# Optimization experiments

Measured on AMD Instinct MI355X. Metric: run time of the kernel, lower is better.

Reference implementation:

```python
import jax, jax.numpy as jnp
import numpy as np


def _chamfer(samp_pc, ref_pc):
    """Squared-L2 chamfer: returns (cost_p1_p2 [B,N], cost_p2_p1 [B,M]).

    samp_pc: [B, N, 3], ref_pc: [B, M, 3]
    """
    s2 = jnp.sum(samp_pc * samp_pc, axis=-1)  # [B, N]
    r2 = jnp.sum(ref_pc * ref_pc, axis=-1)    # [B, M]
    cross = jnp.einsum('bnd,bmd->bnm', samp_pc, ref_pc)  # [B, N, M]
    d2 = s2[:, :, None] + r2[:, None, :] - 2.0 * cross   # [B, N, M]
    d2 = jnp.maximum(d2, 0.0)  # numerical floor
    cost_p1_p2 = jnp.min(d2, axis=2)  # [B, N] nearest ref for each samp point
    cost_p2_p1 = jnp.min(d2, axis=1)  # [B, M] nearest samp for each ref point
    return cost_p1_p2, cost_p2_p1


def setup_inputs() -> dict:
    key = jax.random.key(0)
    k1, k2 = jax.random.split(key)
    B, N, M = 16, 2048, 8192
    ref_pc = jax.random.normal(k1, (B, M, 3), dtype=jnp.float32)
    samp_pc = jax.random.normal(k2, (B, N, 3), dtype=jnp.float32)
    return {"ref_pc": ref_pc, "samp_pc": samp_pc}


def reference(ref_pc, samp_pc):
    cost_p1_p2, cost_p2_p1 = _chamfer(samp_pc, ref_pc)
    cd_p = (jnp.sqrt(cost_p1_p2).mean(axis=1) + jnp.sqrt(cost_p2_p1).mean(axis=1)) / 2.0
    cd_t = cost_p1_p2.mean(axis=1) + cost_p2_p1.mean(axis=1)
    return (cd_p, cd_t)
```

## Files before the change

### kernel.cpp

```cpp
#include <hip/hip_runtime.h>
#include <math.h>

#define BB 16
#define NN 2048
#define MM 8192

#define BLK 256
#define QSPL 2
#define NQ (NN / QSPL)
#define QSTG 256
#define NSTAGE (NQ / QSTG)
#define CTS (QSTG / 32)
#define YB (MM / 256)

typedef __attribute__((ext_vector_type(8))) short short8;
typedef __attribute__((ext_vector_type(16))) float f32x16;

union U16 { uint4 u; short8 s; };

static __device__ __forceinline__ unsigned short f2bf(float f) {
    unsigned int u = __float_as_uint(f);
    unsigned int r = (u + 0x7FFFu + ((u >> 16) & 1u)) >> 16;
    return (unsigned short)r;
}
static __device__ __forceinline__ float bf2f(unsigned short h) {
    return __uint_as_float(((unsigned int)h) << 16);
}

static __device__ __forceinline__ void glds16(const uint4* g, uint4* l) {
    __builtin_amdgcn_global_load_lds(
        (const __attribute__((address_space(1))) unsigned int*)g,
        (__attribute__((address_space(3))) unsigned int*)l,
        16, 0, 0);
}

#define DPP_MIN(v, CTRL)                                                      \
    v = fminf(v, __uint_as_float((unsigned)__builtin_amdgcn_update_dpp(       \
                     0, (int)__float_as_uint(v), CTRL, 0xF, 0xF, true)))
#define SWZ16_MIN(v)                                                          \
    v = fminf(v, __uint_as_float((unsigned)__builtin_amdgcn_ds_swizzle(       \
                     (int)__float_as_uint(v), 0x401F)))


__global__ void __launch_bounds__(BLK) prep_kernel(const float* __restrict__ samp,
                                                   unsigned short* __restrict__ Qpk) {
    const int i = blockIdx.x * BLK + threadIdx.x;
    const float* s0 = samp + (size_t)i * 3;
    float x = s0[0], y = s0[1], z = s0[2];
    float a5[5];
    a5[0] = x; a5[1] = y; a5[2] = z;
    a5[3] = 1.f; a5[4] = fmaf(x, x, fmaf(y, y, z * z));
    unsigned short h[3][5];
#pragma unroll
    for (int j = 0; j < 5; ++j) {
        float v = a5[j];
        h[0][j] = f2bf(v); float r1 = v - bf2f(h[0][j]);
        h[1][j] = f2bf(r1); float r2 = r1 - bf2f(h[1][j]);
        h[2][j] = f2bf(r2);
    }
    const int ordQ[6] = {0, 1, 0, 2, 0, 1};
    unsigned short K[32];
#pragma unroll
    for (int f = 0; f < 2; ++f) {
#pragma unroll
        for (int p2 = 0; p2 < 3; ++p2)
#pragma unroll
            for (int j2 = 0; j2 < 5; ++j2)
                K[f * 16 + p2 * 5 + j2] = h[ordQ[f * 3 + p2]][j2];
        K[f * 16 + 15] = 0;
    }
    unsigned int uu[16];
#pragma unroll
    for (int t = 0; t < 16; ++t)
        uu[t] = (unsigned int)K[2 * t] | ((unsigned int)K[2 * t + 1] << 16);
    uint4* dst = (uint4*)(Qpk + (size_t)i * 32);
    const int sw = (i >> 1) & 3;
    dst[0 ^ sw] = make_uint4(uu[0], uu[1], uu[2], uu[3]);
    dst[1 ^ sw] = make_uint4(uu[4], uu[5], uu[6], uu[7]);
    dst[2 ^ sw] = make_uint4(uu[8], uu[9], uu[10], uu[11]);
    dst[3 ^ sw] = make_uint4(uu[12], uu[13], uu[14], uu[15]);
}

__global__ void __launch_bounds__(BLK, 4) sweep_kernel(const float* __restrict__ ref,
                                                       const unsigned short* __restrict__ Qpk,
                                                       float* __restrict__ ws2p,
                                                       float* __restrict__ ws1p) {
    __shared__ uint4 Qt[2][QSTG * 4];
    __shared__ unsigned int qMin[NQ];

    const int b = blockIdx.x;
    const int m0 = blockIdx.y * 256;
    const int q0 = blockIdx.z * NQ;
    const int tid = threadIdx.x;
    const int w = tid >> 6;
    const int l = tid & 63;
    const int p = l & 31;
    const int kh = l >> 5;

    {
        const float* r0 = ref + ((size_t)(b * MM + m0 + tid)) * 3;
        float x = r0[0], y = r0[1], z = r0[2];
        float a5[5];
        a5[0] = -2.f * x; a5[1] = -2.f * y; a5[2] = -2.f * z;
        a5[3] = fmaf(x, x, fmaf(y, y, z * z)); a5[4] = 1.f;
        unsigned short h[3][5];
#pragma unroll
        for (int j = 0; j < 5; ++j) {
            float v = a5[j];
            h[0][j] = f2bf(v); float r1 = v - bf2f(h[0][j]);
            h[1][j] = f2bf(r1); float r2 = r1 - bf2f(h[1][j]);
            h[2][j] = f2bf(r2);
        }
        const int ordR[6] = {0, 0, 1, 0, 2, 1};
        unsigned short K[32];
#pragma unroll
        for (int f = 0; f < 2; ++f) {
#pragma unroll
            for (int p2 = 0; p2 < 3; ++p2)
#pragma unroll
                for (int j2 = 0; j2 < 5; ++j2)
                    K[f * 16 + p2 * 5 + j2] = h[ordR[f * 3 + p2]][j2];
            K[f * 16 + 15] = 0;
        }
        unsigned int uu[16];
#pragma unroll
        for (int t = 0; t < 16; ++t)
            uu[t] = (unsigned int)K[2 * t] | ((unsigned int)K[2 * t + 1] << 16);
        uint4* scr = &Qt[1][0];
        scr[0 * 256 + tid] = make_uint4(uu[0], uu[1], uu[2], uu[3]);
        scr[1 * 256 + tid] = make_uint4(uu[4], uu[5], uu[6], uu[7]);
        scr[2 * 256 + tid] = make_uint4(uu[8], uu[9], uu[10], uu[11]);
        scr[3 * 256 + tid] = make_uint4(uu[12], uu[13], uu[14], uu[15]);
    }
    for (int i = tid; i < NQ; i += BLK) qMin[i] = 0x7F7F7F7Fu;
    __syncthreads();

    U16 a0f0, a0f1, a1f0, a1f1;
    {
        const uint4* scr = &Qt[1][0];
        a0f0.u = scr[kh * 256 + w * 64 + p];
        a0f1.u = scr[(2 + kh) * 256 + w * 64 + p];
        a1f0.u = scr[kh * 256 + w * 64 + 32 + p];
        a1f1.u = scr[(2 + kh) * 256 + w * 64 + 32 + p];
    }

    const uint4* Q4 = (const uint4*)Qpk + ((size_t)b * NN + q0) * 4;
    {
        uint4* dst = &Qt[0][0];
#pragma unroll
        for (int k = 0; k < 4; ++k) glds16(Q4 + k * BLK + tid, dst + k * BLK + tid);
    }
    __syncthreads();

    float run0[16], run1[16];
#pragma unroll
    for (int j = 0; j < 16; ++j) { run0[j] = INFINITY; run1[j] = INFINITY; }

    const int sw = (p >> 1) & 3;
    const f32x16 fz = {0.f, 0.f, 0.f, 0.f, 0.f, 0.f, 0.f, 0.f,
                       0.f, 0.f, 0.f, 0.f, 0.f, 0.f, 0.f, 0.f};

    for (int st = 0; st < NSTAGE; ++st) {
        const uint4* qb = &Qt[st & 1][0];
        if (st < NSTAGE - 1) {
            const uint4* src = Q4 + (size_t)(st + 1) * (QSTG * 4);
            uint4* dst = &Qt[(st + 1) & 1][0];
#pragma unroll
            for (int k = 0; k < 4; ++k) glds16(src + k * BLK + tid, dst + k * BLK + tid);
        }
#pragma unroll 2
        for (int ct = 0; ct < CTS; ++ct) {
            const int pg = (ct * 32 + p) * 4;
            U16 b0, b1;
            b0.u = qb[pg + (kh ^ sw)];
            b1.u = qb[pg + ((2 + kh) ^ sw)];
            f32x16 d0 = __builtin_amdgcn_mfma_f32_32x32x16_bf16(a0f0.s, b0.s, fz, 0, 0, 0);
            d0 = __builtin_amdgcn_mfma_f32_32x32x16_bf16(a0f1.s, b1.s, d0, 0, 0, 0);
            f32x16 d1 = __builtin_amdgcn_mfma_f32_32x32x16_bf16(a1f0.s, b0.s, fz, 0, 0, 0);
            d1 = __builtin_amdgcn_mfma_f32_32x32x16_bf16(a1f1.s, b1.s, d1, 0, 0, 0);
#pragma unroll
            for (int j = 0; j < 16; ++j) {
                run0[j] = fminf(run0[j], d0[j]);
                run1[j] = fminf(run1[j], d1[j]);
            }
            float tv[8];
#pragma unroll
            for (int k = 0; k < 8; ++k) tv[k] = fminf(d0[k], d0[k + 8]);
#pragma unroll
            for (int k = 0; k < 8; ++k) tv[k] = fminf(tv[k], fminf(d1[k], d1[k + 8]));
#pragma unroll
            for (int k = 0; k < 4; ++k) tv[k] = fminf(tv[k], tv[k + 4]);
            float t = fminf(fminf(tv[0], tv[2]), fminf(tv[1], tv[3]));
            atomicMin(&qMin[st * QSTG + ct * 32 + p], __float_as_uint(fmaxf(t, 0.f)));
        }
        __syncthreads();
    }

    float* w1 = ws1p + ((size_t)blockIdx.y * BB + b) * NN + q0;
#pragma unroll
    for (int i = tid; i < NQ; i += BLK)
        w1[i] = __uint_as_float(qMin[i]);

#pragma unroll
    for (int j = 0; j < 16; ++j) {
        DPP_MIN(run0[j], 0xB1);  DPP_MIN(run0[j], 0x4E);
        DPP_MIN(run0[j], 0x141); DPP_MIN(run0[j], 0x140);
        SWZ16_MIN(run0[j]);
        DPP_MIN(run1[j], 0xB1);  DPP_MIN(run1[j], 0x4E);
        DPP_MIN(run1[j], 0x141); DPP_MIN(run1[j], 0x140);
        SWZ16_MIN(run1[j]);
    }
    float out = 0.f;
#pragma unroll
    for (int j = 0; j < 16; ++j) { if (p == j)      out = run0[j]; }
#pragma unroll
    for (int j = 0; j < 16; ++j) { if (p == 16 + j) out = run1[j]; }
    const int t2 = p >> 4, j4 = p & 15;
    const int row = t2 * 32 + (j4 & 3) + ((j4 >> 2) << 3) + 4 * kh;
    ws2p[((size_t)blockIdx.z * BB + b) * MM + m0 + w * 64 + row] = fmaxf(out, 0.f);
}

#define BLKR 1024
__global__ void __launch_bounds__(BLKR) reduce_kernel(const float* __restrict__ ws1p,
                                                      const float* __restrict__ ws2p,
                                                      float* __restrict__ out) {
    const int b = blockIdx.x;
    const int tid = threadIdx.x;
    const int lane = tid & 63;
    const int wv = tid >> 6;

    float sd1 = 0.f, sr1 = 0.f, sd2 = 0.f, sr2 = 0.f;
#pragma unroll
    for (int i = tid; i < NN; i += BLKR) {
        float m = INFINITY;
#pragma unroll
        for (int y = 0; y < YB; ++y)
            m = fminf(m, ws1p[((size_t)y * BB + b) * NN + i]);
        sd1 += m;
        sr1 += sqrtf(m);
    }
#pragma unroll
    for (int i = tid; i < MM; i += BLKR) {
        float v = fminf(ws2p[(size_t)b * MM + i],
                        ws2p[((size_t)BB + b) * MM + i]);
        sd2 += v;
        sr2 += sqrtf(v);
    }
#pragma unroll
    for (int s = 32; s > 0; s >>= 1) {
        sd1 += __shfl_xor(sd1, s);
        sr1 += __shfl_xor(sr1, s);
        sd2 += __shfl_xor(sd2, s);
        sr2 += __shfl_xor(sr2, s);
    }

    __shared__ float4 red[BLKR / 64];
    if (lane == 0) red[wv] = make_float4(sd1, sr1, sd2, sr2);
    __syncthreads();
    if (tid == 0) {
        float4 acc = red[0];
#pragma unroll
        for (int w = 1; w < BLKR / 64; ++w) {
            acc.x += red[w].x; acc.y += red[w].y;
            acc.z += red[w].z; acc.w += red[w].w;
        }
        out[b]      = (acc.y * (1.0f / NN) + acc.w * (1.0f / MM)) * 0.5f;
        out[BB + b] = acc.x * (1.0f / NN) + acc.z * (1.0f / MM);
    }
}

extern "C" void kernel_launch(void* const* d_in, const int* in_sizes, int n_in,
                              void* d_out, int out_size, void* d_ws, size_t ws_size,
                              hipStream_t stream) {
    const float* ref  = (const float*)d_in[0];
    const float* samp = (const float*)d_in[1];
    float* out = (float*)d_out;

    float* ws2p = (float*)d_ws;
    float* ws1p = ws2p + (size_t)QSPL * BB * MM;
    unsigned short* Qpk = (unsigned short*)(ws1p + (size_t)YB * BB * NN);

    prep_kernel<<<(BB * NN) / BLK, BLK, 0, stream>>>(samp, Qpk);

    dim3 gs(BB, MM / 256, QSPL);
    sweep_kernel<<<gs, BLK, 0, stream>>>(ref, Qpk, ws2p, ws1p);

    reduce_kernel<<<BB, BLKR, 0, stream>>>(ws1p, ws2p, out);
}
```

Measured before the change: 89.18 us.

## Fuse query packing into sweep kernel and split queries four ways

Measured after the change: 89.76 us. Within noise of the previous version (+0.7%).

```diff
diff --git a/kernel.cpp b/kernel.cpp
--- a/kernel.cpp
+++ b/kernel.cpp
@@ -6,11 +6,9 @@
 #define MM 8192
 
 #define BLK 256
-#define QSPL 2
+#define QSPL 4
 #define NQ (NN / QSPL)
-#define QSTG 256
-#define NSTAGE (NQ / QSTG)
-#define CTS (QSTG / 32)
+#define CTS (NQ / 32)
 #define YB (MM / 256)
 
 typedef __attribute__((ext_vector_type(8))) short short8;
@@ -27,11 +25,29 @@
     return __uint_as_float(((unsigned int)h) << 16);
 }
 
-static __device__ __forceinline__ void glds16(const uint4* g, uint4* l) {
-    __builtin_amdgcn_global_load_lds(
-        (const __attribute__((address_space(1))) unsigned int*)g,
-        (__attribute__((address_space(3))) unsigned int*)l,
-        16, 0, 0);
+static __device__ __forceinline__ void pack5(const float a5[5], const int ord[6],
+                                             unsigned int uu[16]) {
+    unsigned short h[3][5];
+#pragma unroll
+    for (int j = 0; j < 5; ++j) {
+        float v = a5[j];
+        h[0][j] = f2bf(v); float r1 = v - bf2f(h[0][j]);
+        h[1][j] = f2bf(r1); float r2 = r1 - bf2f(h[1][j]);
+        h[2][j] = f2bf(r2);
+    }
+    unsigned short K[32];
+#pragma unroll
+    for (int f = 0; f < 2; ++f) {
+#pragma unroll
+        for (int p2 = 0; p2 < 3; ++p2)
+#pragma unroll
+            for (int j2 = 0; j2 < 5; ++j2)
+                K[f * 16 + p2 * 5 + j2] = h[ord[f * 3 + p2]][j2];
+        K[f * 16 + 15] = 0;
+    }
+#pragma unroll
+    for (int t = 0; t < 16; ++t)
+        uu[t] = (unsigned int)K[2 * t] | ((unsigned int)K[2 * t + 1] << 16);
 }
 
 #define DPP_MIN(v, CTRL)                                                      \
@@ -42,50 +58,11 @@
                      (int)__float_as_uint(v), 0x401F)))
 
 
-__global__ void __launch_bounds__(BLK) prep_kernel(const float* __restrict__ samp,
-                                                   unsigned short* __restrict__ Qpk) {
-    const int i = blockIdx.x * BLK + threadIdx.x;
-    const float* s0 = samp + (size_t)i * 3;
-    float x = s0[0], y = s0[1], z = s0[2];
-    float a5[5];
-    a5[0] = x; a5[1] = y; a5[2] = z;
-    a5[3] = 1.f; a5[4] = fmaf(x, x, fmaf(y, y, z * z));
-    unsigned short h[3][5];
-#pragma unroll
-    for (int j = 0; j < 5; ++j) {
-        float v = a5[j];
-        h[0][j] = f2bf(v); float r1 = v - bf2f(h[0][j]);
-        h[1][j] = f2bf(r1); float r2 = r1 - bf2f(h[1][j]);
-        h[2][j] = f2bf(r2);
-    }
-    const int ordQ[6] = {0, 1, 0, 2, 0, 1};
-    unsigned short K[32];
-#pragma unroll
-    for (int f = 0; f < 2; ++f) {
-#pragma unroll
-        for (int p2 = 0; p2 < 3; ++p2)
-#pragma unroll
-            for (int j2 = 0; j2 < 5; ++j2)
-                K[f * 16 + p2 * 5 + j2] = h[ordQ[f * 3 + p2]][j2];
-        K[f * 16 + 15] = 0;
-    }
-    unsigned int uu[16];
-#pragma unroll
-    for (int t = 0; t < 16; ++t)
-        uu[t] = (unsigned int)K[2 * t] | ((unsigned int)K[2 * t + 1] << 16);
-    uint4* dst = (uint4*)(Qpk + (size_t)i * 32);
-    const int sw = (i >> 1) & 3;
-    dst[0 ^ sw] = make_uint4(uu[0], uu[1], uu[2], uu[3]);
-    dst[1 ^ sw] = make_uint4(uu[4], uu[5], uu[6], uu[7]);
-    dst[2 ^ sw] = make_uint4(uu[8], uu[9], uu[10], uu[11]);
-    dst[3 ^ sw] = make_uint4(uu[12], uu[13], uu[14], uu[15]);
-}
-
 __global__ void __launch_bounds__(BLK, 4) sweep_kernel(const float* __restrict__ ref,
-                                                       const unsigned short* __restrict__ Qpk,
+                                                       const float* __restrict__ samp,
                                                        float* __restrict__ ws2p,
                                                        float* __restrict__ ws1p) {
-    __shared__ uint4 Qt[2][QSTG * 4];
+    __shared__ uint4 Qf[4][NQ];
     __shared__ unsigned int qMin[NQ];
 
     const int b = blockIdx.x;
@@ -97,109 +74,84 @@
     const int p = l & 31;
     const int kh = l >> 5;
 
-    {
-        const float* r0 = ref + ((size_t)(b * MM + m0 + tid)) * 3;
-        float x = r0[0], y = r0[1], z = r0[2];
-        float a5[5];
-        a5[0] = -2.f * x; a5[1] = -2.f * y; a5[2] = -2.f * z;
-        a5[3] = fmaf(x, x, fmaf(y, y, z * z)); a5[4] = 1.f;
-        unsigned short h[3][5];
-#pragma unroll
-        for (int j = 0; j < 5; ++j) {
-            float v = a5[j];
-            h[0][j] = f2bf(v); float r1 = v - bf2f(h[0][j]);
-            h[1][j] = f2bf(r1); float r2 = r1 - bf2f(h[1][j]);
-            h[2][j] = f2bf(r2);
-        }
-        const int ordR[6] = {0, 0, 1, 0, 2, 1};
-        unsigned short K[32];
-#pragma unroll
-        for (int f = 0; f < 2; ++f) {
-#pragma unroll
-            for (int p2 = 0; p2 < 3; ++p2)
-#pragma unroll
-                for (int j2 = 0; j2 < 5; ++j2)
-                    K[f * 16 + p2 * 5 + j2] = h[ordR[f * 3 + p2]][j2];
-            K[f * 16 + 15] = 0;
-        }
-        unsigned int uu[16];
-#pragma unroll
-        for (int t = 0; t < 16; ++t)
-            uu[t] = (unsigned int)K[2 * t] | ((unsigned int)K[2 * t + 1] << 16);
-        uint4* scr = &Qt[1][0];
-        scr[0 * 256 + tid] = make_uint4(uu[0], uu[1], uu[2], uu[3]);
-        scr[1 * 256 + tid] = make_uint4(uu[4], uu[5], uu[6], uu[7]);
-        scr[2 * 256 + tid] = make_uint4(uu[8], uu[9], uu[10], uu[11]);
-        scr[3 * 256 + tid] = make_uint4(uu[12], uu[13], uu[14], uu[15]);
-    }
-    for (int i = tid; i < NQ; i += BLK) qMin[i] = 0x7F7F7F7Fu;
-    __syncthreads();
+    const int ordR[6] = {0, 0, 1, 0, 2, 1};
+    const int ordQ[6] = {0, 1, 0, 2, 0, 1};
 
     U16 a0f0, a0f1, a1f0, a1f1;
     {
-        const uint4* scr = &Qt[1][0];
-        a0f0.u = scr[kh * 256 + w * 64 + p];
-        a0f1.u = scr[(2 + kh) * 256 + w * 64 + p];
-        a1f0.u = scr[kh * 256 + w * 64 + 32 + p];
-        a1f1.u = scr[(2 + kh) * 256 + w * 64 + 32 + p];
-    }
-
-    const uint4* Q4 = (const uint4*)Qpk + ((size_t)b * NN + q0) * 4;
-    {
-        uint4* dst = &Qt[0][0];
-#pragma unroll
-        for (int k = 0; k < 4; ++k) glds16(Q4 + k * BLK + tid, dst + k * BLK + tid);
-    }
+        const float* r0 = ref + ((size_t)(b * MM + m0 + w * 64 + p)) * 3;
+        float x = r0[0], y = r0[1], z = r0[2];
+        float a5[5] = {-2.f * x, -2.f * y, -2.f * z, fmaf(x, x, fmaf(y, y, z * z)), 1.f};
+        unsigned int uu[16];
+        pack5(a5, ordR, uu);
+        a0f0.u = kh ? make_uint4(uu[4], uu[5], uu[6], uu[7])
+                    : make_uint4(uu[0], uu[1], uu[2], uu[3]);
+        a0f1.u = kh ? make_uint4(uu[12], uu[13], uu[14], uu[15])
+                    : make_uint4(uu[8], uu[9], uu[10], uu[11]);
+        const float* r1 = r0 + 32 * 3;
+        x = r1[0]; y = r1[1]; z = r1[2];
+        float a6[5] = {-2.f * x, -2.f * y, -2.f * z, fmaf(x, x, fmaf(y, y, z * z)), 1.f};
+        pack5(a6, ordR, uu);
+        a1f0.u = kh ? make_uint4(uu[4], uu[5], uu[6], uu[7])
+                    : make_uint4(uu[0], uu[1], uu[2], uu[3]);
+        a1f1.u = kh ? make_uint4(uu[12], uu[13], uu[14], uu[15])
+                    : make_uint4(uu[8], uu[9], uu[10], uu[11]);
+    }
+
+#pragma unroll
+    for (int k2 = 0; k2 < NQ / BLK; ++k2) {
+        const int q = k2 * BLK + tid;
+        const float* s0 = samp + ((size_t)(b * NN + q0 + q)) * 3;
+        float x = s0[0], y = s0[1], z = s0[2];
+        float a5[5] = {x, y, z, 1.f, fmaf(x, x, fmaf(y, y, z * z))};
+        unsigned int uu[16];
+        pack5(a5, ordQ, uu);
+        Qf[0][q] = make_uint4(uu[0], uu[1], uu[2], uu[3]);
+        Qf[1][q] = make_uint4(uu[4], uu[5], uu[6], uu[7]);
+        Qf[2][q] = make_uint4(uu[8], uu[9], uu[10], uu[11]);
+        Qf[3][q] = make_uint4(uu[12], uu[13], uu[14], uu[15]);
+    }
+    qMin[tid] = 0x7F7F7F7Fu;
+    qMin[tid + BLK] = 0x7F7F7F7Fu;
     __syncthreads();
 
     float run0[16], run1[16];
 #pragma unroll
     for (int j = 0; j < 16; ++j) { run0[j] = INFINITY; run1[j] = INFINITY; }
 
-    const int sw = (p >> 1) & 3;
     const f32x16 fz = {0.f, 0.f, 0.f, 0.f, 0.f, 0.f, 0.f, 0.f,
                        0.f, 0.f, 0.f, 0.f, 0.f, 0.f, 0.f, 0.f};
 
-    for (int st = 0; st < NSTAGE; ++st) {
-        const uint4* qb = &Qt[st & 1][0];
-        if (st < NSTAGE - 1) {
-            const uint4* src = Q4 + (size_t)(st + 1) * (QSTG * 4);
-            uint4* dst = &Qt[(st + 1) & 1][0];
-#pragma unroll
-            for (int k = 0; k < 4; ++k) glds16(src + k * BLK + tid, dst + k * BLK + tid);
+#pragma unroll 2
+    for (int ct = 0; ct < CTS; ++ct) {
+        const int q = ct * 32 + p;
+        U16 b0, b1;
+        b0.u = Qf[kh][q];
+        b1.u = Qf[2 + kh][q];
+        f32x16 d0 = __builtin_amdgcn_mfma_f32_32x32x16_bf16(a0f0.s, b0.s, fz, 0, 0, 0);
+        d0 = __builtin_amdgcn_mfma_f32_32x32x16_bf16(a0f1.s, b1.s, d0, 0, 0, 0);
+        f32x16 d1 = __builtin_amdgcn_mfma_f32_32x32x16_bf16(a1f0.s, b0.s, fz, 0, 0, 0);
+        d1 = __builtin_amdgcn_mfma_f32_32x32x16_bf16(a1f1.s, b1.s, d1, 0, 0, 0);
+#pragma unroll
+        for (int j = 0; j < 16; ++j) {
+            run0[j] = fminf(run0[j], d0[j]);
+            run1[j] = fminf(run1[j], d1[j]);
         }
-#pragma unroll 2
-        for (int ct = 0; ct < CTS; ++ct) {
-            const int pg = (ct * 32 + p) * 4;
-            U16 b0, b1;
-            b0.u = qb[pg + (kh ^ sw)];
-            b1.u = qb[pg + ((2 + kh) ^ sw)];
-            f32x16 d0 = __builtin_amdgcn_mfma_f32_32x32x16_bf16(a0f0.s, b0.s, fz, 0, 0, 0);
-            d0 = __builtin_amdgcn_mfma_f32_32x32x16_bf16(a0f1.s, b1.s, d0, 0, 0, 0);
-            f32x16 d1 = __builtin_amdgcn_mfma_f32_32x32x16_bf16(a1f0.s, b0.s, fz, 0, 0, 0);
-            d1 = __builtin_amdgcn_mfma_f32_32x32x16_bf16(a1f1.s, b1.s, d1, 0, 0, 0);
-#pragma unroll
-            for (int j = 0; j < 16; ++j) {
-                run0[j] = fminf(run0[j], d0[j]);
-                run1[j] = fminf(run1[j], d1[j]);
-            }
-            float tv[8];
-#pragma unroll
-            for (int k = 0; k < 8; ++k) tv[k] = fminf(d0[k], d0[k + 8]);
-#pragma unroll
-            for (int k = 0; k < 8; ++k) tv[k] = fminf(tv[k], fminf(d1[k], d1[k + 8]));
-#pragma unroll
-            for (int k = 0; k < 4; ++k) tv[k] = fminf(tv[k], tv[k + 4]);
-            float t = fminf(fminf(tv[0], tv[2]), fminf(tv[1], tv[3]));
-            atomicMin(&qMin[st * QSTG + ct * 32 + p], __float_as_uint(fmaxf(t, 0.f)));
-        }
-        __syncthreads();
-    }
+        float tv[8];
+#pragma unroll
+        for (int k = 0; k < 8; ++k) tv[k] = fminf(d0[k], d0[k + 8]);
+#pragma unroll
+        for (int k = 0; k < 8; ++k) tv[k] = fminf(tv[k], fminf(d1[k], d1[k + 8]));
+#pragma unroll
+        for (int k = 0; k < 4; ++k) tv[k] = fminf(tv[k], tv[k + 4]);
+        float t = fminf(fminf(tv[0], tv[2]), fminf(tv[1], tv[3]));
+        atomicMin(&qMin[q], __float_as_uint(fmaxf(t, 0.f)));
+    }
+    __syncthreads();
 
     float* w1 = ws1p + ((size_t)blockIdx.y * BB + b) * NN + q0;
-#pragma unroll
-    for (int i = tid; i < NQ; i += BLK)
-        w1[i] = __uint_as_float(qMin[i]);
+    w1[tid] = __uint_as_float(qMin[tid]);
+    w1[tid + BLK] = __uint_as_float(qMin[tid + BLK]);
 
 #pragma unroll
     for (int j = 0; j < 16; ++j) {
@@ -241,8 +193,10 @@
     }
 #pragma unroll
     for (int i = tid; i < MM; i += BLKR) {
-        float v = fminf(ws2p[(size_t)b * MM + i],
-                        ws2p[((size_t)BB + b) * MM + i]);
+        float v = INFINITY;
+#pragma unroll
+        for (int zz = 0; zz < QSPL; ++zz)
+            v = fminf(v, ws2p[((size_t)zz * BB + b) * MM + i]);
         sd2 += v;
         sr2 += sqrtf(v);
     }
@@ -278,12 +232,9 @@
 
     float* ws2p = (float*)d_ws;
     float* ws1p = ws2p + (size_t)QSPL * BB * MM;
-    unsigned short* Qpk = (unsigned short*)(ws1p + (size_t)YB * BB * NN);
-
-    prep_kernel<<<(BB * NN) / BLK, BLK, 0, stream>>>(samp, Qpk);
 
     dim3 gs(BB, MM / 256, QSPL);
-    sweep_kernel<<<gs, BLK, 0, stream>>>(ref, Qpk, ws2p, ws1p);
+    sweep_kernel<<<gs, BLK, 0, stream>>>(ref, samp, ws2p, ws1p);
 
     reduce_kernel<<<BB, BLKR, 0, stream>>>(ws1p, ws2p, out);
 }
```
